# Kernel optimization log

Measured on AMD Instinct MI355X. Metric: run time of the kernel, lower is better.

The kernel has to match this reference:

```python
import jax, jax.numpy as jnp
import numpy as np

B, T, C = 2, 2048, 1024
H, D = 16, 64
F = 4096
EPS = 1e-5


def _layernorm(x, scale, shift):
    mean = jnp.mean(x, axis=-1, keepdims=True)
    var = jnp.mean((x - mean) ** 2, axis=-1, keepdims=True)  # unbiased=False
    return scale * (x - mean) * jax.lax.rsqrt(var + EPS) + shift


def setup_inputs() -> dict:
    key = jax.random.key(0)
    ks = jax.random.split(key, 16)
    s = lambda k, shape, fan_in: jax.random.normal(k, shape, jnp.float32) * (1.0 / np.sqrt(fan_in))
    return {
        "x": jax.random.normal(ks[0], (B, T, C), jnp.float32),
        # weights stored [in, out] so y = x @ W + b (same math as torch Linear)
        "Wq": s(ks[1], (C, H * D), C), "bq": jnp.zeros((H * D,), jnp.float32),
        "Wk": s(ks[2], (C, H * D), C), "bk": jnp.zeros((H * D,), jnp.float32),
        "Wv": s(ks[3], (C, H * D), C), "bv": jnp.zeros((H * D,), jnp.float32),
        "Wo": s(ks[4], (H * D, C), H * D), "bo": jnp.zeros((C,), jnp.float32),
        "W1": s(ks[5], (C, F), C), "b1": jnp.zeros((F,), jnp.float32),
        "W2": s(ks[6], (F, C), F), "b2": jnp.zeros((C,), jnp.float32),
        "ln1_scale": jnp.ones((C,), jnp.float32), "ln1_shift": jnp.zeros((C,), jnp.float32),
        "ln2_scale": jnp.ones((C,), jnp.float32), "ln2_shift": jnp.zeros((C,), jnp.float32),
    }


def reference(x, Wq, bq, Wk, bk, Wv, bv, Wo, bo, W1, b1, W2, b2,
              ln1_scale, ln1_shift, ln2_scale, ln2_shift):
    b, t, c = x.shape
    # --- attention sub-block ---
    h = _layernorm(x, ln1_scale, ln1_shift)
    q = (h @ Wq + bq).reshape(b, t, H, D)
    k = (h @ Wk + bk).reshape(b, t, H, D)
    v = (h @ Wv + bv).reshape(b, t, H, D)
    scores = jnp.einsum('bqhd,bkhd->bhqk', q, k)  # [B,H,T,T]
    causal = jnp.tril(jnp.ones((t, t), dtype=bool))
    scores = jnp.where(causal, scores, -jnp.inf)
    attn = jax.nn.softmax(scores / np.sqrt(D), axis=-1)
    ctx = jnp.einsum('bhqk,bkhd->bqhd', attn, v).reshape(b, t, H * D)
    x = x + (ctx @ Wo + bo)  # drop_rate=0 -> dropout is identity
    # --- MLP sub-block ---
    h = _layernorm(x, ln2_scale, ln2_shift)
    h = jax.nn.gelu(h @ W1 + b1, approximate=False)
    x = x + (h @ W2 + b2)
    return x
```

## Files before the change

kernel.cpp:

```cpp
#include <hip/hip_runtime.h>
#include <hip/hip_bf16.h>
#include <stdint.h>

#define B_ 2
#define T_ 2048
#define C_ 1024
#define H_ 16
#define D_ 64
#define F_ 4096
#define M_ (B_*T_)

typedef unsigned short ushort_t;
typedef __attribute__((ext_vector_type(8))) short short8;
typedef __attribute__((ext_vector_type(4))) float f32x4;

__device__ __forceinline__ float bf2f(ushort_t u) {
    union { unsigned u; float f; } c; c.u = ((unsigned)u) << 16; return c.f;
}
__device__ __forceinline__ ushort_t f2bf(float f) {
    union { float f; unsigned u; } c; c.f = f;
    unsigned u = c.u;
    unsigned r = (u + 0x7FFFu + ((u >> 16) & 1u)) >> 16;
    return (ushort_t)r;
}

__device__ __forceinline__ float fexp2(float x) { return __builtin_amdgcn_exp2f(x); }

__device__ __forceinline__ void async16(void* lds, const void* g) {
    __builtin_amdgcn_global_load_lds(
        (const __attribute__((address_space(1))) unsigned int*)(uintptr_t)g,
        (__attribute__((address_space(3))) unsigned int*)(uintptr_t)lds,
        16, 0, 0);
}

__global__ void transpose_cast_k(const float* __restrict__ in, ushort_t* __restrict__ out,
                                 int R, int C) {
    __shared__ ushort_t tile[32][33];
    int tx = threadIdx.x, ty = threadIdx.y;
    int x = blockIdx.x * 32 + tx;
    int y0 = blockIdx.y * 32;
#pragma unroll
    for (int i = 0; i < 32; i += 8)
        tile[ty + i][tx] = f2bf(in[(size_t)(y0 + ty + i) * C + x]);
    __syncthreads();
    int x2 = y0 + tx;
    int y2 = blockIdx.x * 32;
#pragma unroll
    for (int i = 0; i < 32; i += 8)
        out[(size_t)(y2 + ty + i) * R + x2] = tile[tx][ty + i];
}

__global__ void transpose_bf_k(const ushort_t* __restrict__ in, ushort_t* __restrict__ out,
                               int R, int C) {
    __shared__ ushort_t tile[32][33];
    int tx = threadIdx.x, ty = threadIdx.y;
    int x = blockIdx.x * 32 + tx;
    int y0 = blockIdx.y * 32;
#pragma unroll
    for (int i = 0; i < 32; i += 8)
        tile[ty + i][tx] = in[(size_t)(y0 + ty + i) * C + x];
    __syncthreads();
    int x2 = y0 + tx;
    int y2 = blockIdx.x * 32;
#pragma unroll
    for (int i = 0; i < 32; i += 8)
        out[(size_t)(y2 + ty + i) * R + x2] = tile[tx][ty + i];
}

__global__ __launch_bounds__(256) void ln_kernel(const float* __restrict__ xin,
                                                 const float* __restrict__ scale_p,
                                                 const float* __restrict__ shift_p,
                                                 ushort_t* __restrict__ out) {
    int row = blockIdx.x, t = threadIdx.x;
    int wv = t >> 6, lane = t & 63;
    const float* xr = xin + (size_t)row * 1024 + t * 4;
    float4 v = *(const float4*)xr;
    float f[4] = {v.x, v.y, v.z, v.w};
    float s = f[0] + f[1] + f[2] + f[3];
    float q = f[0]*f[0] + f[1]*f[1] + f[2]*f[2] + f[3]*f[3];
#pragma unroll
    for (int off = 1; off < 64; off <<= 1) {
        s += __shfl_xor(s, off, 64);
        q += __shfl_xor(q, off, 64);
    }
    __shared__ float sh_s[4], sh_q[4];
    if (lane == 0) { sh_s[wv] = s; sh_q[wv] = q; }
    __syncthreads();
    float S = sh_s[0] + sh_s[1] + sh_s[2] + sh_s[3];
    float Q = sh_q[0] + sh_q[1] + sh_q[2] + sh_q[3];
    float mean = S * (1.0f / 1024.0f);
    float var = Q * (1.0f / 1024.0f) - mean * mean;
    float rstd = rsqrtf(var + 1e-5f);
    float4 scv = *(const float4*)(scale_p + t * 4);
    float4 shv = *(const float4*)(shift_p + t * 4);
    ushort4 o;
    o.x = f2bf((f[0] - mean) * rstd * scv.x + shv.x);
    o.y = f2bf((f[1] - mean) * rstd * scv.y + shv.y);
    o.z = f2bf((f[2] - mean) * rstd * scv.z + shv.z);
    o.w = f2bf((f[3] - mean) * rstd * scv.w + shv.w);
    *(ushort4*)(out + (size_t)row * 1024 + t * 4) = o;
}

template <int MT, int EPI>
__global__ __launch_bounds__(256) void gemm_bt(const ushort_t* __restrict__ A,
                                               const ushort_t* __restrict__ Bt,
                                               const float* __restrict__ b0,
                                               const float* __restrict__ b1,
                                               const float* __restrict__ b2,
                                               const float* __restrict__ res,
                                               void* __restrict__ out0,
                                               void* __restrict__ out1,
                                               void* __restrict__ out2,
                                               int M, int N, int K) {
    __shared__ ushort_t As[32 * MT * 32];
    __shared__ ushort_t Bs[128 * 32];
    const int t = threadIdx.x;
    const int wv = t >> 6, lane = t & 63, lo = lane & 15, hi = lane >> 4;
    const int wr = wv >> 1, wc = wv & 1;
    const int mb = blockIdx.y, nb = blockIdx.x;

    f32x4 acc[MT][4];
#pragma unroll
    for (int i = 0; i < MT; ++i)
#pragma unroll
        for (int j = 0; j < 4; ++j) acc[i][j] = (f32x4){0.f, 0.f, 0.f, 0.f};

    for (int k0 = 0; k0 < K; k0 += 32) {
#pragma unroll
        for (int i = 0; i < MT / 2; ++i) {
            int c = i * 256 + t;
            int row = c >> 2, kc = c & 3;
            async16((char*)As + (size_t)(i * 256 + wv * 64) * 16,
                    A + (size_t)(mb * 32 * MT + row) * K + k0 + kc * 8);
        }
#pragma unroll
        for (int i = 0; i < 2; ++i) {
            int c = i * 256 + t;
            int row = c >> 2, kc = c & 3;
            async16((char*)Bs + (size_t)(i * 256 + wv * 64) * 16,
                    Bt + (size_t)(nb * 128 + row) * K + k0 + kc * 8);
        }
        __syncthreads();

        short8 af[MT], bfr[4];
#pragma unroll
        for (int mi = 0; mi < MT; ++mi)
            af[mi] = *(const short8*)(As + (wr * 16 * MT + mi * 16 + lo) * 32 + hi * 8);
#pragma unroll
        for (int ni = 0; ni < 4; ++ni)
            bfr[ni] = *(const short8*)(Bs + (wc * 64 + ni * 16 + lo) * 32 + hi * 8);
#pragma unroll
        for (int mi = 0; mi < MT; ++mi)
#pragma unroll
            for (int ni = 0; ni < 4; ++ni)
                acc[mi][ni] = __builtin_amdgcn_mfma_f32_16x16x32_bf16(
                    af[mi], bfr[ni], acc[mi][ni], 0, 0, 0);
        __syncthreads();
    }

#pragma unroll
    for (int ni = 0; ni < 4; ++ni) {
        int n = nb * 128 + wc * 64 + ni * 16 + lo;
        float bn;
        ushort_t* obf = nullptr;
        int coln = n;
        if (EPI == 3) {
            int seg = n >> 10; coln = n & 1023;
            bn = (seg == 0 ? b0 : seg == 1 ? b1 : b2)[coln];
            obf = (ushort_t*)(seg == 0 ? out0 : seg == 1 ? out1 : out2);
        } else {
            bn = b0[n];
        }
#pragma unroll
        for (int mi = 0; mi < MT; ++mi) {
#pragma unroll
            for (int r = 0; r < 4; ++r) {
                int m = mb * 32 * MT + wr * 16 * MT + mi * 16 + 4 * hi + r;
                float v = acc[mi][ni][r] + bn;
                if (EPI == 1) {
                    size_t idx = (size_t)m * N + n;
                    ((float*)out0)[idx] = v + res[idx];
                } else if (EPI == 2) {
                    v = 0.5f * v * (1.0f + erff(v * 0.70710678118654752f));
                    ((ushort_t*)out0)[(size_t)m * N + n] = f2bf(v);
                } else {
                    obf[(size_t)m * 1024 + coln] = f2bf(v);
                }
            }
        }
    }
}

__global__ __launch_bounds__(256) void attn_kernel(const ushort_t* __restrict__ q,
                                                   const ushort_t* __restrict__ k,
                                                   const ushort_t* __restrict__ vt,
                                                   ushort_t* __restrict__ ctx) {
    __shared__ ushort_t Ks[2][64 * 64];
    __shared__ ushort_t VTs[2][64 * 64];
    __shared__ ushort_t Ps[8][16 * 72];

    const int t = threadIdx.x;
    const int wv = t >> 6, lane = t & 63, lo = lane & 15, hi = lane >> 4;
    const int qb = (int)gridDim.x - 1 - (int)blockIdx.x;
    const int bh = blockIdx.y, b = bh >> 4, h = bh & 15;
    const int q0 = qb * 128;
    const size_t headoff = (size_t)h * 64;
    const size_t rowbase = (size_t)b * T_ * 1024;
    const ushort_t* vbase = vt + headoff * (size_t)M_ + (size_t)b * T_;

    short8 qf[2][2];
#pragma unroll
    for (int g = 0; g < 2; ++g) {
        const ushort_t* qp = q + rowbase + (size_t)(q0 + g * 64 + wv * 16 + lo) * 1024 + headoff;
        qf[g][0] = *(const short8*)(qp + hi * 8);
        qf[g][1] = *(const short8*)(qp + 32 + hi * 8);
    }

    float m_g[2], l_g[2];
    f32x4 o_acc[2][4];
#pragma unroll
    for (int g = 0; g < 2; ++g) {
        m_g[g] = -1e30f; l_g[g] = 0.f;
#pragma unroll
        for (int dt = 0; dt < 4; ++dt) o_acc[g][dt] = (f32x4){0.f, 0.f, 0.f, 0.f};
    }

    const int ktmax = 2 * qb + 1;
    const float SC = 0.18033688011112042f;

    auto stage = [&](int bb, int kt) {
        const int k0 = kt * 64;
#pragma unroll
        for (int i = 0; i < 2; ++i) {
            int c = i * 256 + t;
            int row = c >> 3, c8 = c & 7;
            int gsw = c8 ^ (row & 7);
            async16((char*)&Ks[bb][0] + (size_t)(i * 256 + wv * 64) * 16,
                    k + rowbase + (size_t)(k0 + row) * 1024 + headoff + gsw * 8);
            async16((char*)&VTs[bb][0] + (size_t)(i * 256 + wv * 64) * 16,
                    vbase + (size_t)row * M_ + k0 + gsw * 8);
        }
    };

    stage(0, 0);
    for (int kt = 0; kt <= ktmax; ++kt) {
        const int bb = kt & 1;
        const int k0 = kt * 64;
        __syncthreads();
        if (kt < ktmax) stage(bb ^ 1, kt + 1);

        short8 pf[2][2];
        int any_g[2];
#pragma unroll
        for (int g = 0; g < 2; ++g) {
            const int qg0 = q0 + g * 64 + wv * 16;
            const int diff = qg0 - k0;
            any_g[g] = (diff >= 0);
            if (!any_g[g]) continue;
            const int cmax = diff >= 48 ? 3 : (diff >> 4);

            f32x4 sacc[4];
#pragma unroll
            for (int kt16 = 0; kt16 < 4; ++kt16) {
                if (kt16 <= cmax) {
                    int row = kt16 * 16 + lo, sw = row & 7;
                    short8 kf0 = *(const short8*)(&Ks[bb][0] + row * 64 + (hi ^ sw) * 8);
                    short8 kf1 = *(const short8*)(&Ks[bb][0] + row * 64 + ((4 + hi) ^ sw) * 8);
                    f32x4 z = (f32x4){0.f, 0.f, 0.f, 0.f};
                    z = __builtin_amdgcn_mfma_f32_16x16x32_bf16(kf0, qf[g][0], z, 0, 0, 0);
                    z = __builtin_amdgcn_mfma_f32_16x16x32_bf16(kf1, qf[g][1], z, 0, 0, 0);
#pragma unroll
                    for (int r = 0; r < 4; ++r) sacc[kt16][r] = z[r] * SC;
                } else {
                    sacc[kt16] = (f32x4){-1e30f, -1e30f, -1e30f, -1e30f};
                }
            }
            if (diff < 64) {
                const int qrow = qg0 + lo;
#pragma unroll
                for (int r = 0; r < 4; ++r) {
                    int key = k0 + cmax * 16 + 4 * hi + r;
                    if (key > qrow) sacc[cmax][r] = -1e30f;
                }
            }

            float mx = -1e30f;
#pragma unroll
            for (int kt16 = 0; kt16 < 4; ++kt16)
#pragma unroll
                for (int r = 0; r < 4; ++r) mx = fmaxf(mx, sacc[kt16][r]);
            mx = fmaxf(mx, __shfl_xor(mx, 16, 64));
            mx = fmaxf(mx, __shfl_xor(mx, 32, 64));
            float mnew = fmaxf(m_g[g], mx);
            float alpha = fexp2(m_g[g] - mnew);
            m_g[g] = mnew;

            ushort_t* Pw = Ps[wv * 2 + g];
            float rs = 0.f;
#pragma unroll
            for (int kt16 = 0; kt16 < 4; ++kt16)
#pragma unroll
                for (int r = 0; r < 4; ++r) {
                    float p = fexp2(sacc[kt16][r] - mnew);
                    rs += p;
                    Pw[lo * 72 + kt16 * 16 + 4 * hi + r] = f2bf(p);
                }
            rs += __shfl_xor(rs, 16, 64);
            rs += __shfl_xor(rs, 32, 64);
            l_g[g] = l_g[g] * alpha + rs;

#pragma unroll
            for (int r = 0; r < 4; ++r) {
                float ab = __shfl(alpha, 4 * hi + r, 64);
#pragma unroll
                for (int dt = 0; dt < 4; ++dt) o_acc[g][dt][r] *= ab;
            }

            pf[g][0] = *(const short8*)(Pw + lo * 72 + hi * 8);
            pf[g][1] = *(const short8*)(Pw + lo * 72 + 32 + hi * 8);
        }

#pragma unroll
        for (int dt = 0; dt < 4; ++dt) {
            int row = dt * 16 + lo, sw = row & 7;
            short8 vf0 = *(const short8*)(&VTs[bb][0] + row * 64 + (hi ^ sw) * 8);
            short8 vf1 = *(const short8*)(&VTs[bb][0] + row * 64 + ((4 + hi) ^ sw) * 8);
#pragma unroll
            for (int g = 0; g < 2; ++g) {
                if (!any_g[g]) continue;
                o_acc[g][dt] = __builtin_amdgcn_mfma_f32_16x16x32_bf16(pf[g][0], vf0, o_acc[g][dt], 0, 0, 0);
                o_acc[g][dt] = __builtin_amdgcn_mfma_f32_16x16x32_bf16(pf[g][1], vf1, o_acc[g][dt], 0, 0, 0);
            }
        }
    }

#pragma unroll
    for (int g = 0; g < 2; ++g) {
#pragma unroll
        for (int r = 0; r < 4; ++r) {
            float lb = __shfl(l_g[g], 4 * hi + r, 64);
            float inv = 1.0f / lb;
            size_t row = rowbase + (size_t)(q0 + g * 64 + wv * 16 + 4 * hi + r) * 1024 + headoff;
#pragma unroll
            for (int dt = 0; dt < 4; ++dt)
                ctx[row + dt * 16 + lo] = f2bf(o_acc[g][dt][r] * inv);
        }
    }
}

extern "C" void kernel_launch(void* const* d_in, const int* in_sizes, int n_in,
                              void* d_out, int out_size, void* d_ws, size_t ws_size,
                              hipStream_t stream) {
    (void)in_sizes; (void)n_in; (void)out_size; (void)ws_size;
    const float* x    = (const float*)d_in[0];
    const float* Wq   = (const float*)d_in[1];
    const float* bq   = (const float*)d_in[2];
    const float* Wk   = (const float*)d_in[3];
    const float* bk   = (const float*)d_in[4];
    const float* Wv   = (const float*)d_in[5];
    const float* bv   = (const float*)d_in[6];
    const float* Wo   = (const float*)d_in[7];
    const float* bo   = (const float*)d_in[8];
    const float* W1   = (const float*)d_in[9];
    const float* b1   = (const float*)d_in[10];
    const float* W2   = (const float*)d_in[11];
    const float* b2   = (const float*)d_in[12];
    const float* ln1s = (const float*)d_in[13];
    const float* ln1b = (const float*)d_in[14];
    const float* ln2s = (const float*)d_in[15];
    const float* ln2b = (const float*)d_in[16];

    char* ws = (char*)d_ws;
    const size_t MB = 1024 * 1024;
    ushort_t* wqkv = (ushort_t*)(ws + 0 * MB);
    ushort_t* wtq  = (ushort_t*)(ws + 0 * MB);
    ushort_t* wtk  = (ushort_t*)(ws + 2 * MB);
    ushort_t* wtv  = (ushort_t*)(ws + 4 * MB);
    ushort_t* wto  = (ushort_t*)(ws + 6 * MB);
    ushort_t* wt1  = (ushort_t*)(ws + 8 * MB);
    ushort_t* wt2  = (ushort_t*)(ws + 16 * MB);
    ushort_t* hbuf = (ushort_t*)(ws + 24 * MB);
    ushort_t* qb_  = (ushort_t*)(ws + 32 * MB);
    ushort_t* kb_  = (ushort_t*)(ws + 40 * MB);
    ushort_t* vb_  = (ushort_t*)(ws + 48 * MB);
    ushort_t* ctx  = (ushort_t*)(ws + 56 * MB);
    ushort_t* hid  = (ushort_t*)(ws + 32 * MB);
    float*    x1   = (float*)(ws + 64 * MB);
    ushort_t* vtb  = (ushort_t*)(ws + 64 * MB);

    dim3 tb(32, 8);
    transpose_cast_k<<<dim3(32, 32), tb, 0, stream>>>(Wq, wtq, 1024, 1024);
    transpose_cast_k<<<dim3(32, 32), tb, 0, stream>>>(Wk, wtk, 1024, 1024);
    transpose_cast_k<<<dim3(32, 32), tb, 0, stream>>>(Wv, wtv, 1024, 1024);
    transpose_cast_k<<<dim3(32, 32), tb, 0, stream>>>(Wo, wto, 1024, 1024);
    transpose_cast_k<<<dim3(128, 32), tb, 0, stream>>>(W1, wt1, 1024, 4096);
    transpose_cast_k<<<dim3(32, 128), tb, 0, stream>>>(W2, wt2, 4096, 1024);

    ln_kernel<<<4096, 256, 0, stream>>>(x, ln1s, ln1b, hbuf);

    gemm_bt<4, 3><<<dim3(24, 32), 256, 0, stream>>>(hbuf, wqkv, bq, bk, bv, nullptr,
                                                    qb_, kb_, vb_, 4096, 3072, 1024);

    transpose_bf_k<<<dim3(32, 128), tb, 0, stream>>>(vb_, vtb, 4096, 1024);

    attn_kernel<<<dim3(16, 32), 256, 0, stream>>>(qb_, kb_, vtb, ctx);

    gemm_bt<2, 1><<<dim3(8, 64), 256, 0, stream>>>(ctx, wto, bo, nullptr, nullptr, x,
                                                   x1, nullptr, nullptr, 4096, 1024, 1024);

    ln_kernel<<<4096, 256, 0, stream>>>(x1, ln2s, ln2b, hbuf);

    gemm_bt<4, 2><<<dim3(32, 32), 256, 0, stream>>>(hbuf, wt1, b1, nullptr, nullptr, nullptr,
                                                    hid, nullptr, nullptr, 4096, 4096, 1024);

    gemm_bt<2, 1><<<dim3(8, 64), 256, 0, stream>>>(hid, wt2, b2, nullptr, nullptr, x1,
                                                   (float*)d_out, nullptr, nullptr, 4096, 1024, 4096);
}
```

Before: 456.9 us.

## Merge weight transposes into one launch and write V transposed from QKV GEMM

The six weight transpose-cast launches become one kernel that picks its source matrix from the block index. The QKV GEMM epilogue now writes the V segment straight into the transposed layout with packed 4-element stores, which removes the separate V transpose kernel and its round trip through global memory. The attention softmax is moved into a lambda and the causal mask uses offsets relative to the tile; neither changes the maths. The transposed V stores are strided by M, so their coalescing differs from the row-major Q and K stores.

After: 439.9 us. -3.7%, faster.

```diff
diff --git a/kernel.cpp b/kernel.cpp
--- a/kernel.cpp
+++ b/kernel.cpp
@@ -33,35 +33,37 @@
         16, 0, 0);
 }
 
-__global__ void transpose_cast_k(const float* __restrict__ in, ushort_t* __restrict__ out,
-                                 int R, int C) {
+__global__ __launch_bounds__(256) void transpose_all_k(
+    const float* __restrict__ Wq, const float* __restrict__ Wk,
+    const float* __restrict__ Wv, const float* __restrict__ Wo,
+    const float* __restrict__ W1, const float* __restrict__ W2,
+    ushort_t* __restrict__ oq, ushort_t* __restrict__ ok,
+    ushort_t* __restrict__ ov, ushort_t* __restrict__ oo,
+    ushort_t* __restrict__ o1, ushort_t* __restrict__ o2) {
     __shared__ ushort_t tile[32][33];
+    int id = blockIdx.x;
+    const float* in; ushort_t* out; int R, Cc, bx, by;
+    if (id < 4096) {
+        int w = id >> 10, loc = id & 1023;
+        in  = w == 0 ? Wq : w == 1 ? Wk : w == 2 ? Wv : Wo;
+        out = w == 0 ? oq : w == 1 ? ok : w == 2 ? ov : oo;
+        R = 1024; Cc = 1024; bx = loc & 31; by = loc >> 5;
+    } else if (id < 8192) {
+        int loc = id - 4096; in = W1; out = o1; R = 1024; Cc = 4096;
+        bx = loc & 127; by = loc >> 7;
+    } else {
+        int loc = id - 8192; in = W2; out = o2; R = 4096; Cc = 1024;
+        bx = loc & 31; by = loc >> 5;
+    }
     int tx = threadIdx.x, ty = threadIdx.y;
-    int x = blockIdx.x * 32 + tx;
-    int y0 = blockIdx.y * 32;
+    int x = bx * 32 + tx;
+    int y0 = by * 32;
 #pragma unroll
     for (int i = 0; i < 32; i += 8)
-        tile[ty + i][tx] = f2bf(in[(size_t)(y0 + ty + i) * C + x]);
+        tile[ty + i][tx] = f2bf(in[(size_t)(y0 + ty + i) * Cc + x]);
     __syncthreads();
     int x2 = y0 + tx;
-    int y2 = blockIdx.x * 32;
-#pragma unroll
-    for (int i = 0; i < 32; i += 8)
-        out[(size_t)(y2 + ty + i) * R + x2] = tile[tx][ty + i];
-}
-
-__global__ void transpose_bf_k(const ushort_t* __restrict__ in, ushort_t* __restrict__ out,
-                               int R, int C) {
-    __shared__ ushort_t tile[32][33];
-    int tx = threadIdx.x, ty = threadIdx.y;
-    int x = blockIdx.x * 32 + tx;
-    int y0 = blockIdx.y * 32;
-#pragma unroll
-    for (int i = 0; i < 32; i += 8)
-        tile[ty + i][tx] = in[(size_t)(y0 + ty + i) * C + x];
-    __syncthreads();
-    int x2 = y0 + tx;
-    int y2 = blockIdx.x * 32;
+    int y2 = bx * 32;
 #pragma unroll
     for (int i = 0; i < 32; i += 8)
         out[(size_t)(y2 + ty + i) * R + x2] = tile[tx][ty + i];
@@ -163,28 +165,38 @@
         int n = nb * 128 + wc * 64 + ni * 16 + lo;
         float bn;
         ushort_t* obf = nullptr;
-        int coln = n;
+        int coln = n, seg = 0;
         if (EPI == 3) {
-            int seg = n >> 10; coln = n & 1023;
+            seg = n >> 10; coln = n & 1023;
             bn = (seg == 0 ? b0 : seg == 1 ? b1 : b2)[coln];
-            obf = (ushort_t*)(seg == 0 ? out0 : seg == 1 ? out1 : out2);
+            obf = (ushort_t*)(seg == 0 ? out0 : out1);
         } else {
             bn = b0[n];
         }
 #pragma unroll
         for (int mi = 0; mi < MT; ++mi) {
-#pragma unroll
-            for (int r = 0; r < 4; ++r) {
-                int m = mb * 32 * MT + wr * 16 * MT + mi * 16 + 4 * hi + r;
-                float v = acc[mi][ni][r] + bn;
-                if (EPI == 1) {
-                    size_t idx = (size_t)m * N + n;
-                    ((float*)out0)[idx] = v + res[idx];
-                } else if (EPI == 2) {
-                    v = 0.5f * v * (1.0f + erff(v * 0.70710678118654752f));
-                    ((ushort_t*)out0)[(size_t)m * N + n] = f2bf(v);
-                } else {
-                    obf[(size_t)m * 1024 + coln] = f2bf(v);
+            if (EPI == 3 && seg == 2) {
+                int m0 = mb * 32 * MT + wr * 16 * MT + mi * 16 + 4 * hi;
+                ushort4 pk;
+                pk.x = f2bf(acc[mi][ni][0] + bn);
+                pk.y = f2bf(acc[mi][ni][1] + bn);
+                pk.z = f2bf(acc[mi][ni][2] + bn);
+                pk.w = f2bf(acc[mi][ni][3] + bn);
+                *(ushort4*)((ushort_t*)out2 + (size_t)coln * M + m0) = pk;
+            } else {
+#pragma unroll
+                for (int r = 0; r < 4; ++r) {
+                    int m = mb * 32 * MT + wr * 16 * MT + mi * 16 + 4 * hi + r;
+                    float v = acc[mi][ni][r] + bn;
+                    if (EPI == 1) {
+                        size_t idx = (size_t)m * N + n;
+                        ((float*)out0)[idx] = v + res[idx];
+                    } else if (EPI == 2) {
+                        v = 0.5f * v * (1.0f + erff(v * 0.70710678118654752f));
+                        ((ushort_t*)out0)[(size_t)m * N + n] = f2bf(v);
+                    } else {
+                        obf[(size_t)m * 1024 + coln] = f2bf(v);
+                    }
                 }
             }
         }
@@ -227,18 +239,52 @@
 
     const int ktmax = 2 * qb + 1;
     const float SC = 0.18033688011112042f;
+    const f32x4 NEG4 = (f32x4){-1e30f, -1e30f, -1e30f, -1e30f};
 
     auto stage = [&](int bb, int kt) {
-        const int k0 = kt * 64;
+        const int k0s = kt * 64;
 #pragma unroll
         for (int i = 0; i < 2; ++i) {
             int c = i * 256 + t;
             int row = c >> 3, c8 = c & 7;
             int gsw = c8 ^ (row & 7);
             async16((char*)&Ks[bb][0] + (size_t)(i * 256 + wv * 64) * 16,
-                    k + rowbase + (size_t)(k0 + row) * 1024 + headoff + gsw * 8);
+                    k + rowbase + (size_t)(k0s + row) * 1024 + headoff + gsw * 8);
             async16((char*)&VTs[bb][0] + (size_t)(i * 256 + wv * 64) * 16,
-                    vbase + (size_t)row * M_ + k0 + gsw * 8);
+                    vbase + (size_t)row * M_ + k0s + gsw * 8);
+        }
+    };
+
+    auto softmax_g = [&](f32x4* sacc, int gi) {
+        float mx = -1e30f;
+#pragma unroll
+        for (int kt16 = 0; kt16 < 4; ++kt16)
+#pragma unroll
+            for (int r = 0; r < 4; ++r) mx = fmaxf(mx, sacc[kt16][r]);
+        mx = fmaxf(mx, __shfl_xor(mx, 16, 64));
+        mx = fmaxf(mx, __shfl_xor(mx, 32, 64));
+        float mnew = fmaxf(m_g[gi], mx);
+        float alpha = fexp2(m_g[gi] - mnew);
+        m_g[gi] = mnew;
+        ushort_t* Pw = Ps[wv * 2 + gi];
+        float rs = 0.f;
+#pragma unroll
+        for (int kt16 = 0; kt16 < 4; ++kt16) {
+#pragma unroll
+            for (int r = 0; r < 4; ++r) {
+                float p = fexp2(sacc[kt16][r] - mnew);
+                rs += p;
+                Pw[lo * 72 + kt16 * 16 + 4 * hi + r] = f2bf(p);
+            }
+        }
+        rs += __shfl_xor(rs, 16, 64);
+        rs += __shfl_xor(rs, 32, 64);
+        l_g[gi] = l_g[gi] * alpha + rs;
+#pragma unroll
+        for (int r = 0; r < 4; ++r) {
+            float ab = __shfl(alpha, 4 * hi + r, 64);
+#pragma unroll
+            for (int dt = 0; dt < 4; ++dt) o_acc[gi][dt][r] *= ab;
         }
     };
 
@@ -272,52 +318,22 @@
 #pragma unroll
                     for (int r = 0; r < 4; ++r) sacc[kt16][r] = z[r] * SC;
                 } else {
-                    sacc[kt16] = (f32x4){-1e30f, -1e30f, -1e30f, -1e30f};
+                    sacc[kt16] = NEG4;
                 }
             }
             if (diff < 64) {
-                const int qrow = qg0 + lo;
+                const int qrow = diff + lo;
 #pragma unroll
                 for (int r = 0; r < 4; ++r) {
-                    int key = k0 + cmax * 16 + 4 * hi + r;
+                    int key = cmax * 16 + 4 * hi + r;
                     if (key > qrow) sacc[cmax][r] = -1e30f;
                 }
             }
 
-            float mx = -1e30f;
-#pragma unroll
-            for (int kt16 = 0; kt16 < 4; ++kt16)
-#pragma unroll
-                for (int r = 0; r < 4; ++r) mx = fmaxf(mx, sacc[kt16][r]);
-            mx = fmaxf(mx, __shfl_xor(mx, 16, 64));
-            mx = fmaxf(mx, __shfl_xor(mx, 32, 64));
-            float mnew = fmaxf(m_g[g], mx);
-            float alpha = fexp2(m_g[g] - mnew);
-            m_g[g] = mnew;
-
-            ushort_t* Pw = Ps[wv * 2 + g];
-            float rs = 0.f;
-#pragma unroll
-            for (int kt16 = 0; kt16 < 4; ++kt16)
-#pragma unroll
-                for (int r = 0; r < 4; ++r) {
-                    float p = fexp2(sacc[kt16][r] - mnew);
-                    rs += p;
-                    Pw[lo * 72 + kt16 * 16 + 4 * hi + r] = f2bf(p);
-                }
-            rs += __shfl_xor(rs, 16, 64);
-            rs += __shfl_xor(rs, 32, 64);
-            l_g[g] = l_g[g] * alpha + rs;
-
-#pragma unroll
-            for (int r = 0; r < 4; ++r) {
-                float ab = __shfl(alpha, 4 * hi + r, 64);
-#pragma unroll
-                for (int dt = 0; dt < 4; ++dt) o_acc[g][dt][r] *= ab;
-            }
-
-            pf[g][0] = *(const short8*)(Pw + lo * 72 + hi * 8);
-            pf[g][1] = *(const short8*)(Pw + lo * 72 + 32 + hi * 8);
+            softmax_g(sacc, g);
+
+            pf[g][0] = *(const short8*)(Ps[wv * 2 + g] + lo * 72 + hi * 8);
+            pf[g][1] = *(const short8*)(Ps[wv * 2 + g] + lo * 72 + 32 + hi * 8);
         }
 
 #pragma unroll
@@ -382,26 +398,18 @@
     ushort_t* hbuf = (ushort_t*)(ws + 24 * MB);
     ushort_t* qb_  = (ushort_t*)(ws + 32 * MB);
     ushort_t* kb_  = (ushort_t*)(ws + 40 * MB);
-    ushort_t* vb_  = (ushort_t*)(ws + 48 * MB);
     ushort_t* ctx  = (ushort_t*)(ws + 56 * MB);
     ushort_t* hid  = (ushort_t*)(ws + 32 * MB);
     float*    x1   = (float*)(ws + 64 * MB);
     ushort_t* vtb  = (ushort_t*)(ws + 64 * MB);
 
-    dim3 tb(32, 8);
-    transpose_cast_k<<<dim3(32, 32), tb, 0, stream>>>(Wq, wtq, 1024, 1024);
-    transpose_cast_k<<<dim3(32, 32), tb, 0, stream>>>(Wk, wtk, 1024, 1024);
-    transpose_cast_k<<<dim3(32, 32), tb, 0, stream>>>(Wv, wtv, 1024, 1024);
-    transpose_cast_k<<<dim3(32, 32), tb, 0, stream>>>(Wo, wto, 1024, 1024);
-    transpose_cast_k<<<dim3(128, 32), tb, 0, stream>>>(W1, wt1, 1024, 4096);
-    transpose_cast_k<<<dim3(32, 128), tb, 0, stream>>>(W2, wt2, 4096, 1024);
+    transpose_all_k<<<12288, dim3(32, 8), 0, stream>>>(Wq, Wk, Wv, Wo, W1, W2,
+                                                       wtq, wtk, wtv, wto, wt1, wt2);
 
     ln_kernel<<<4096, 256, 0, stream>>>(x, ln1s, ln1b, hbuf);
 
     gemm_bt<4, 3><<<dim3(24, 32), 256, 0, stream>>>(hbuf, wqkv, bq, bk, bv, nullptr,
-                                                    qb_, kb_, vb_, 4096, 3072, 1024);
-
-    transpose_bf_k<<<dim3(32, 128), tb, 0, stream>>>(vb_, vtb, 4096, 1024);
+                                                    qb_, kb_, vtb, 4096, 3072, 1024);
 
     attn_kernel<<<dim3(16, 32), 256, 0, stream>>>(qb_, kb_, vtb, ctx);
 
```
